# Performance work log

Measured on AMD Instinct MI355X. Metric: run time of the kernel, lower is better.

The kernel has to match this reference:

```python
import jax, jax.numpy as jnp
import numpy as np

NUM_HEADS = 8
NUM_POINTS = 4


def setup_inputs() -> dict:
    key = jax.random.key(0)
    ks = jax.random.split(key, 8)
    N, H, W, E = 4, 32, 32, 256
    L = H * W
    query = jax.random.normal(ks[0], (N, H, W, E), jnp.float32)
    reference_points = jax.random.uniform(ks[1], (N, L, 2), dtype=jnp.float32)
    # params stored as [in, out] so y = x @ W + b (same math as torch Linear)
    W_off = jax.random.normal(ks[2], (E, NUM_HEADS * NUM_POINTS * 2), jnp.float32) * 0.01
    b_off = jnp.zeros((NUM_HEADS * NUM_POINTS * 2,), jnp.float32)
    W_attn = jax.random.normal(ks[3], (E, NUM_HEADS * NUM_POINTS), jnp.float32) * 0.02
    b_attn = jnp.zeros((NUM_HEADS * NUM_POINTS,), jnp.float32)
    W_out = jax.random.normal(ks[4], (E, E), jnp.float32) * 0.02
    b_out = jnp.zeros((E,), jnp.float32)
    return {"query": query, "reference_points": reference_points,
            "W_off": W_off, "b_off": b_off, "W_attn": W_attn, "b_attn": b_attn,
            "W_out": W_out, "b_out": b_out}


def reference(query, reference_points, W_off, b_off, W_attn, b_attn, W_out, b_out):
    N, Hh, Ww, E = query.shape
    L = Hh * Ww
    q = query.reshape(N, L, E)
    # sampling offsets: [N, heads, L, P, 2]
    offs = (q @ W_off + b_off).reshape(N, L, NUM_HEADS, NUM_POINTS, 2).transpose(0, 2, 1, 3, 4)
    # attention weights, softmax over points: [N, heads, L, P]
    attn = jax.nn.softmax((q @ W_attn + b_attn).reshape(N, L, NUM_HEADS, NUM_POINTS).transpose(0, 2, 1, 3), axis=-1)
    # sampling locations in [0,1], mapped to grid_sample's [-1,1]
    grid = (reference_points[:, None, :, None, :] + offs) * 2.0 - 1.0  # [N,h,L,P,2]
    # align_corners=False pixel coords: ((g+1)*size - 1) / 2
    x = (grid[..., 0] + 1.0) * Ww * 0.5 - 0.5
    y = (grid[..., 1] + 1.0) * Hh * 0.5 - 0.5
    x0 = jnp.floor(x)
    y0 = jnp.floor(y)
    wx1 = x - x0
    wy1 = y - y0
    x0i = x0.astype(jnp.int32)
    y0i = y0.astype(jnp.int32)
    qflat = query.transpose(0, 3, 1, 2).reshape(N, E, L)  # [N, E, H*W]

    def corner(xi, yi, w):
        # zeros padding: out-of-range taps contribute 0
        valid = (xi >= 0) & (xi < Ww) & (yi >= 0) & (yi < Hh)
        idx = jnp.clip(yi, 0, Hh - 1) * Ww + jnp.clip(xi, 0, Ww - 1)  # [N,h,L,P]
        g = jax.vmap(lambda qf, i: qf[:, i])(qflat, idx.reshape(N, -1))  # [N,E,h*L*P]
        g = g.reshape(N, E, NUM_HEADS, L, NUM_POINTS)
        return g * (w * valid)[:, None]  # broadcast over E

    sampled = (corner(x0i, y0i, (1.0 - wx1) * (1.0 - wy1))
               + corner(x0i + 1, y0i, wx1 * (1.0 - wy1))
               + corner(x0i, y0i + 1, (1.0 - wx1) * wy1)
               + corner(x0i + 1, y0i + 1, wx1 * wy1))  # [N,E,h,L,P]
    # weighted sum over points, mean over heads
    out = jnp.einsum('nehlp,nhlp->nle', sampled, attn) / NUM_HEADS
    out = out.reshape(N, Hh, Ww, E) @ W_out + b_out
    return out
```

## Files before the change

kernel.cpp:

```cpp
#include <hip/hip_runtime.h>

#define NHEADS 8
#define NPTS 4
#define EDIM 256
#define GRIDW 32
#define LTOK 1024
#define NTOK 4096

__global__ __launch_bounds__(512) void fused_all_kernel(
    const float* __restrict__ query,
    const float* __restrict__ refp,
    const float* __restrict__ W_off,
    const float* __restrict__ b_off,
    const float* __restrict__ W_attn,
    const float* __restrict__ b_attn,
    const float* __restrict__ W_outp,
    const float* __restrict__ b_out,
    float* __restrict__ out)
{
    const int tb = blockIdx.x * 8;
    const int tid = threadIdx.x;
    const int lane = tid & 63;
    const int wv = tid >> 6;

    __shared__ float qs[8][260];
    __shared__ float lg[8][96];
    __shared__ float cw[8][128];
    __shared__ int   ci[8][128];
    __shared__ float ps[8192];

    {
        const int kb = __builtin_amdgcn_readfirstlane(wv * 32);
        const int colA = lane & 31;
        float a[8] = {};
        float b[8] = {};
        #pragma unroll 2
        for (int kk = 0; kk < 32; kk += 4) {
            const int k = kb + kk;
            const float w0 = W_off[(k + 0) * 64 + lane];
            const float w1 = W_off[(k + 1) * 64 + lane];
            const float w2 = W_off[(k + 2) * 64 + lane];
            const float w3 = W_off[(k + 3) * 64 + lane];
            const float v0 = W_attn[(k + 0) * 32 + colA];
            const float v1 = W_attn[(k + 1) * 32 + colA];
            const float v2 = W_attn[(k + 2) * 32 + colA];
            const float v3 = W_attn[(k + 3) * 32 + colA];
            #pragma unroll
            for (int t = 0; t < 8; ++t) {
                const float4 q4 = *(const float4*)&query[(tb + t) * EDIM + k];
                a[t] = fmaf(q4.x, w0, a[t]);
                a[t] = fmaf(q4.y, w1, a[t]);
                a[t] = fmaf(q4.z, w2, a[t]);
                a[t] = fmaf(q4.w, w3, a[t]);
                b[t] = fmaf(q4.x, v0, b[t]);
                b[t] = fmaf(q4.y, v1, b[t]);
                b[t] = fmaf(q4.z, v2, b[t]);
                b[t] = fmaf(q4.w, v3, b[t]);
            }
        }
        #pragma unroll
        for (int t = 0; t < 8; ++t) ps[(wv * 8 + t) * 64 + lane] = a[t];
        if (lane < 32) {
            #pragma unroll
            for (int t = 0; t < 8; ++t) ps[4096 + (wv * 8 + t) * 32 + lane] = b[t];
        }
    }
    __syncthreads();

    {
        float s = b_off[lane];
        #pragma unroll
        for (int k = 0; k < 8; ++k) s += ps[(k * 8 + wv) * 64 + lane];
        lg[wv][lane] = s;
    }
    if (tid < 256) {
        const int t = tid >> 5;
        const int col = tid & 31;
        float s = b_attn[col];
        #pragma unroll
        for (int k = 0; k < 8; ++k) s += ps[4096 + (k * 8 + t) * 32 + col];
        lg[t][64 + col] = s;
    }
    __syncthreads();

    if (tid < 256) {
        const int t = tid >> 5;
        const int s = tid & 31;
        const int token = tb + t;
        const int n = token >> 10;
        const int h = s >> 2;
        const float l0 = lg[t][64 + h * 4 + 0];
        const float l1 = lg[t][64 + h * 4 + 1];
        const float l2 = lg[t][64 + h * 4 + 2];
        const float l3 = lg[t][64 + h * 4 + 3];
        const float m  = fmaxf(fmaxf(l0, l1), fmaxf(l2, l3));
        const float denom = __expf(l0 - m) + __expf(l1 - m) + __expf(l2 - m) + __expf(l3 - m);
        const float aw = __expf(lg[t][64 + s] - m) / (denom * (float)NHEADS);

        const float rx = refp[token * 2 + 0];
        const float ry = refp[token * 2 + 1];
        const float x = (rx + lg[t][2 * s + 0]) * 32.0f - 0.5f;
        const float y = (ry + lg[t][2 * s + 1]) * 32.0f - 0.5f;
        const float x0f = floorf(x);
        const float y0f = floorf(y);
        const float wx = x - x0f;
        const float wy = y - y0f;
        const int x0 = (int)x0f;
        const int y0 = (int)y0f;

        const int xi[4] = { x0, x0 + 1, x0, x0 + 1 };
        const int yi[4] = { y0, y0, y0 + 1, y0 + 1 };
        const float wc[4] = { (1.f - wx) * (1.f - wy), wx * (1.f - wy),
                              (1.f - wx) * wy,         wx * wy };
        #pragma unroll
        for (int c = 0; c < 4; ++c) {
            const bool valid = (xi[c] >= 0) & (xi[c] < GRIDW) & (yi[c] >= 0) & (yi[c] < GRIDW);
            cw[t][s * 4 + c] = valid ? (wc[c] * aw) : 0.f;
            ci[t][s * 4 + c] = valid ? ((n * LTOK + yi[c] * GRIDW + xi[c]) * EDIM) : 0;
        }
    }
    __syncthreads();

    {
        const int loff = lane * 4;
        const int   ciA = ci[wv][lane];
        const int   ciB = ci[wv][64 + lane];
        const float cwA = cw[wv][lane];
        const float cwB = cw[wv][64 + lane];

        float4 acc0 = {0.f, 0.f, 0.f, 0.f};
        float4 acc1 = {0.f, 0.f, 0.f, 0.f};
        float4 acc2 = {0.f, 0.f, 0.f, 0.f};
        float4 acc3 = {0.f, 0.f, 0.f, 0.f};

        #pragma unroll
        for (int t = 0; t < 64; ++t) {
            const int sidx = __builtin_amdgcn_readlane(ciA, t);
            const float wt = __int_as_float(__builtin_amdgcn_readlane(__float_as_int(cwA), t));
            const float4 v = *(const float4*)&query[sidx + loff];
            float4& acc = (t & 2) ? ((t & 1) ? acc3 : acc2) : ((t & 1) ? acc1 : acc0);
            acc.x = fmaf(wt, v.x, acc.x);
            acc.y = fmaf(wt, v.y, acc.y);
            acc.z = fmaf(wt, v.z, acc.z);
            acc.w = fmaf(wt, v.w, acc.w);
        }
        #pragma unroll
        for (int t = 0; t < 64; ++t) {
            const int sidx = __builtin_amdgcn_readlane(ciB, t);
            const float wt = __int_as_float(__builtin_amdgcn_readlane(__float_as_int(cwB), t));
            const float4 v = *(const float4*)&query[sidx + loff];
            float4& acc = (t & 2) ? ((t & 1) ? acc3 : acc2) : ((t & 1) ? acc1 : acc0);
            acc.x = fmaf(wt, v.x, acc.x);
            acc.y = fmaf(wt, v.y, acc.y);
            acc.z = fmaf(wt, v.z, acc.z);
            acc.w = fmaf(wt, v.w, acc.w);
        }

        float4 acc;
        acc.x = (acc0.x + acc1.x) + (acc2.x + acc3.x);
        acc.y = (acc0.y + acc1.y) + (acc2.y + acc3.y);
        acc.z = (acc0.z + acc1.z) + (acc2.z + acc3.z);
        acc.w = (acc0.w + acc1.w) + (acc2.w + acc3.w);
        *(float4*)&qs[wv][loff] = acc;
    }
    __syncthreads();

    {
        const int kbase = wv * 32;
        const int c0 = lane * 4;

        float4 acc[8];
        #pragma unroll
        for (int r = 0; r < 8; ++r) acc[r] = float4{0.f, 0.f, 0.f, 0.f};

        #pragma unroll 2
        for (int kk = 0; kk < 32; kk += 4) {
            const int k = kbase + kk;
            const float4 w0 = *(const float4*)&W_outp[(k + 0) * EDIM + c0];
            const float4 w1 = *(const float4*)&W_outp[(k + 1) * EDIM + c0];
            const float4 w2 = *(const float4*)&W_outp[(k + 2) * EDIM + c0];
            const float4 w3 = *(const float4*)&W_outp[(k + 3) * EDIM + c0];
            #pragma unroll
            for (int r = 0; r < 8; ++r) {
                const float4 a = *(const float4*)&qs[r][k];
                acc[r].x = fmaf(a.x, w0.x, acc[r].x);
                acc[r].y = fmaf(a.x, w0.y, acc[r].y);
                acc[r].z = fmaf(a.x, w0.z, acc[r].z);
                acc[r].w = fmaf(a.x, w0.w, acc[r].w);
                acc[r].x = fmaf(a.y, w1.x, acc[r].x);
                acc[r].y = fmaf(a.y, w1.y, acc[r].y);
                acc[r].z = fmaf(a.y, w1.z, acc[r].z);
                acc[r].w = fmaf(a.y, w1.w, acc[r].w);
                acc[r].x = fmaf(a.z, w2.x, acc[r].x);
                acc[r].y = fmaf(a.z, w2.y, acc[r].y);
                acc[r].z = fmaf(a.z, w2.z, acc[r].z);
                acc[r].w = fmaf(a.z, w2.w, acc[r].w);
                acc[r].x = fmaf(a.w, w3.x, acc[r].x);
                acc[r].y = fmaf(a.w, w3.y, acc[r].y);
                acc[r].z = fmaf(a.w, w3.z, acc[r].z);
                acc[r].w = fmaf(a.w, w3.w, acc[r].w);
            }
        }

        if (wv >= 4) {
            const int base = (wv - 4) * 2048;
            #pragma unroll
            for (int r = 0; r < 8; ++r)
                *(float4*)&ps[base + r * 256 + c0] = acc[r];
        }
        __syncthreads();
        if (wv < 4) {
            const int base = wv * 2048;
            #pragma unroll
            for (int r = 0; r < 8; ++r) {
                float4 p = *(const float4*)&ps[base + r * 256 + c0];
                p.x += acc[r].x; p.y += acc[r].y;
                p.z += acc[r].z; p.w += acc[r].w;
                *(float4*)&ps[base + r * 256 + c0] = p;
            }
        }
        __syncthreads();
    }

    {
        const int c0 = lane * 4;
        const float4 s0 = *(const float4*)&ps[0 * 2048 + wv * 256 + c0];
        const float4 s1 = *(const float4*)&ps[1 * 2048 + wv * 256 + c0];
        const float4 s2 = *(const float4*)&ps[2 * 2048 + wv * 256 + c0];
        const float4 s3 = *(const float4*)&ps[3 * 2048 + wv * 256 + c0];
        const float4 bb = *(const float4*)&b_out[c0];
        float4 o;
        o.x = ((s0.x + s1.x) + (s2.x + s3.x)) + bb.x;
        o.y = ((s0.y + s1.y) + (s2.y + s3.y)) + bb.y;
        o.z = ((s0.z + s1.z) + (s2.z + s3.z)) + bb.z;
        o.w = ((s0.w + s1.w) + (s2.w + s3.w)) + bb.w;
        *(float4*)&out[(tb + wv) * EDIM + c0] = o;
    }
}

extern "C" void kernel_launch(void* const* d_in, const int* in_sizes, int n_in,
                              void* d_out, int out_size, void* d_ws, size_t ws_size,
                              hipStream_t stream) {
    const float* query  = (const float*)d_in[0];
    const float* refp   = (const float*)d_in[1];
    const float* W_off  = (const float*)d_in[2];
    const float* b_off  = (const float*)d_in[3];
    const float* W_attn = (const float*)d_in[4];
    const float* b_attn = (const float*)d_in[5];
    const float* W_out  = (const float*)d_in[6];
    const float* b_out  = (const float*)d_in[7];
    float* out = (float*)d_out;

    fused_all_kernel<<<NTOK / 8, 512, 0, stream>>>(query, refp, W_off, b_off,
                                                   W_attn, b_attn, W_out, b_out, out);
}
```

Measured before the change: 33.42 us.

## Gather sampled values from an fp16 copy of query and broadcast output-projection inputs via readlane

Adds a pre-pass kernel that converts the query tensor to fp16 in the workspace, so the bilinear gather loop reads 8 bytes per lane instead of 16, which halves gather traffic. The output projection now keeps each wave's 32 activation columns in registers and broadcasts them with readlane instead of doing repeated LDS float4 reads. The cost is an extra kernel launch plus a full read and write pass over query, and reduced precision in the sampled values.

```diff
diff --git a/kernel.cpp b/kernel.cpp
--- a/kernel.cpp
+++ b/kernel.cpp
@@ -1,4 +1,5 @@
 #include <hip/hip_runtime.h>
+#include <hip/hip_fp16.h>
 
 #define NHEADS 8
 #define NPTS 4
@@ -7,8 +8,23 @@
 #define LTOK 1024
 #define NTOK 4096
 
+__global__ __launch_bounds__(256) void cvt_kernel(
+    const float* __restrict__ q,
+    __half* __restrict__ qh)
+{
+    const int i = blockIdx.x * 256 + threadIdx.x;
+    const float4 v = *(const float4*)&q[i * 4];
+    const __half2 h0 = __floats2half2_rn(v.x, v.y);
+    const __half2 h1 = __floats2half2_rn(v.z, v.w);
+    uint2 u;
+    u.x = *(const unsigned int*)&h0;
+    u.y = *(const unsigned int*)&h1;
+    *(uint2*)&qh[i * 4] = u;
+}
+
 __global__ __launch_bounds__(512) void fused_all_kernel(
     const float* __restrict__ query,
+    const __half* __restrict__ qh,
     const float* __restrict__ refp,
     const float* __restrict__ W_off,
     const float* __restrict__ b_off,
@@ -137,23 +153,27 @@
         for (int t = 0; t < 64; ++t) {
             const int sidx = __builtin_amdgcn_readlane(ciA, t);
             const float wt = __int_as_float(__builtin_amdgcn_readlane(__float_as_int(cwA), t));
-            const float4 v = *(const float4*)&query[sidx + loff];
+            const uint2 u = *(const uint2*)&qh[sidx + loff];
+            const float2 f0 = __half22float2(*(const __half2*)&u.x);
+            const float2 f1 = __half22float2(*(const __half2*)&u.y);
             float4& acc = (t & 2) ? ((t & 1) ? acc3 : acc2) : ((t & 1) ? acc1 : acc0);
-            acc.x = fmaf(wt, v.x, acc.x);
-            acc.y = fmaf(wt, v.y, acc.y);
-            acc.z = fmaf(wt, v.z, acc.z);
-            acc.w = fmaf(wt, v.w, acc.w);
+            acc.x = fmaf(wt, f0.x, acc.x);
+            acc.y = fmaf(wt, f0.y, acc.y);
+            acc.z = fmaf(wt, f1.x, acc.z);
+            acc.w = fmaf(wt, f1.y, acc.w);
         }
         #pragma unroll
         for (int t = 0; t < 64; ++t) {
             const int sidx = __builtin_amdgcn_readlane(ciB, t);
             const float wt = __int_as_float(__builtin_amdgcn_readlane(__float_as_int(cwB), t));
-            const float4 v = *(const float4*)&query[sidx + loff];
+            const uint2 u = *(const uint2*)&qh[sidx + loff];
+            const float2 f0 = __half22float2(*(const __half2*)&u.x);
+            const float2 f1 = __half22float2(*(const __half2*)&u.y);
             float4& acc = (t & 2) ? ((t & 1) ? acc3 : acc2) : ((t & 1) ? acc1 : acc0);
-            acc.x = fmaf(wt, v.x, acc.x);
-            acc.y = fmaf(wt, v.y, acc.y);
-            acc.z = fmaf(wt, v.z, acc.z);
-            acc.w = fmaf(wt, v.w, acc.w);
+            acc.x = fmaf(wt, f0.x, acc.x);
+            acc.y = fmaf(wt, f0.y, acc.y);
+            acc.z = fmaf(wt, f1.x, acc.z);
+            acc.w = fmaf(wt, f1.y, acc.w);
         }
 
         float4 acc;
@@ -169,36 +189,25 @@
         const int kbase = wv * 32;
         const int c0 = lane * 4;
 
+        float areg[8];
+        #pragma unroll
+        for (int r = 0; r < 8; ++r) areg[r] = qs[r][kbase + (lane & 31)];
+
         float4 acc[8];
         #pragma unroll
         for (int r = 0; r < 8; ++r) acc[r] = float4{0.f, 0.f, 0.f, 0.f};
 
-        #pragma unroll 2
-        for (int kk = 0; kk < 32; kk += 4) {
-            const int k = kbase + kk;
-            const float4 w0 = *(const float4*)&W_outp[(k + 0) * EDIM + c0];
-            const float4 w1 = *(const float4*)&W_outp[(k + 1) * EDIM + c0];
-            const float4 w2 = *(const float4*)&W_outp[(k + 2) * EDIM + c0];
-            const float4 w3 = *(const float4*)&W_outp[(k + 3) * EDIM + c0];
+        #pragma unroll
+        for (int kk = 0; kk < 32; ++kk) {
+            const float4 w = *(const float4*)&W_outp[(kbase + kk) * EDIM + c0];
             #pragma unroll
             for (int r = 0; r < 8; ++r) {
-                const float4 a = *(const float4*)&qs[r][k];
-                acc[r].x = fmaf(a.x, w0.x, acc[r].x);
-                acc[r].y = fmaf(a.x, w0.y, acc[r].y);
-                acc[r].z = fmaf(a.x, w0.z, acc[r].z);
-                acc[r].w = fmaf(a.x, w0.w, acc[r].w);
-                acc[r].x = fmaf(a.y, w1.x, acc[r].x);
-                acc[r].y = fmaf(a.y, w1.y, acc[r].y);
-                acc[r].z = fmaf(a.y, w1.z, acc[r].z);
-                acc[r].w = fmaf(a.y, w1.w, acc[r].w);
-                acc[r].x = fmaf(a.z, w2.x, acc[r].x);
-                acc[r].y = fmaf(a.z, w2.y, acc[r].y);
-                acc[r].z = fmaf(a.z, w2.z, acc[r].z);
-                acc[r].w = fmaf(a.z, w2.w, acc[r].w);
-                acc[r].x = fmaf(a.w, w3.x, acc[r].x);
-                acc[r].y = fmaf(a.w, w3.y, acc[r].y);
-                acc[r].z = fmaf(a.w, w3.z, acc[r].z);
-                acc[r].w = fmaf(a.w, w3.w, acc[r].w);
+                const float a = __int_as_float(
+                    __builtin_amdgcn_readlane(__float_as_int(areg[r]), kk));
+                acc[r].x = fmaf(a, w.x, acc[r].x);
+                acc[r].y = fmaf(a, w.y, acc[r].y);
+                acc[r].z = fmaf(a, w.z, acc[r].z);
+                acc[r].w = fmaf(a, w.w, acc[r].w);
             }
         }
 
@@ -251,6 +260,9 @@
     const float* b_out  = (const float*)d_in[7];
     float* out = (float*)d_out;
 
-    fused_all_kernel<<<NTOK / 8, 512, 0, stream>>>(query, refp, W_off, b_off,
+    __half* qh = (__half*)d_ws;
+
+    cvt_kernel<<<NTOK * EDIM / 4 / 256, 256, 0, stream>>>(query, qh);
+    fused_all_kernel<<<NTOK / 8, 512, 0, stream>>>(query, qh, refp, W_off, b_off,
                                                    W_attn, b_attn, W_out, b_out, out);
 }
```

Measured after the change: 39.65 us. +18.6%, slower.
